# Performance work log

Measured on AMD Instinct MI355X. Metric: run time of the kernel, lower is better.

## Reference

```python
import jax, jax.numpy as jnp
import numpy as np

N = 4096        # batch nodes
E = 65536       # random edges (self-loops appended -> 69632 total)
F_IN = 256
H = 128
C = 2
MIN = 1024      # minority (class 1) count; first MIN nodes
REP = 2         # int(N_pct/100) synthetic reps per minority sample


def setup_inputs() -> dict:
    key = jax.random.key(0)
    ks = jax.random.split(key, 24)
    feat = jax.random.normal(ks[0], (N, F_IN), dtype=jnp.float32)
    src = jax.random.randint(ks[1], (E,), 0, N, dtype=jnp.int32)
    dst = jax.random.randint(ks[2], (E,), 0, N, dtype=jnp.int32)
    loops = jnp.arange(N, dtype=jnp.int32)
    src = jnp.concatenate([src, loops])
    dst = jnp.concatenate([dst, loops])
    # dense batch adjacency (target for EdgeLoss), A[i,j]=1 if edge j->i
    adj = jnp.zeros((N, N), dtype=jnp.float32).at[dst, src].set(1.0)
    # deterministic labels: first MIN nodes are minority class 1
    labels = jnp.concatenate([jnp.ones((MIN,), jnp.int32), jnp.zeros((N - MIN,), jnp.int32)])

    def w(k, shape, fan_in):
        return jax.random.normal(k, shape, dtype=jnp.float32) / np.sqrt(fan_in)

    params = dict(
        W_pool0=w(ks[3], (F_IN, F_IN), F_IN), b_pool0=jnp.zeros((F_IN,), jnp.float32),
        W_self0=w(ks[4], (H, F_IN), F_IN), W_neigh0=w(ks[5], (H, F_IN), F_IN), b0=jnp.zeros((H,), jnp.float32),
        W_pool1=w(ks[6], (H, H), H), b_pool1=jnp.zeros((H,), jnp.float32),
        W_self1=w(ks[7], (H, H), H), W_neigh1=w(ks[8], (H, H), H), b1=jnp.zeros((H,), jnp.float32),
        de_weight=jax.random.uniform(ks[9], (H, H), jnp.float32, -1.0 / np.sqrt(H), 1.0 / np.sqrt(H)),
        W_conv=w(ks[10], (H, 2 * H), 2 * H),
        W_clf=w(ks[11], (C, H), H), b_clf=jnp.zeros((C,), jnp.float32),
        gaps=jax.random.uniform(ks[12], (MIN, REP), jnp.float32),  # SMOTE interpolation gaps
    )
    return dict(feat=feat, adj=adj, src=src, dst=dst, labels=labels, **params)


def _sage_pool_layer(h, src, dst, W_pool, b_pool, W_self, W_neigh, b):
    # DGL SAGEConv aggregator_type='pool': max over neighbors of relu(fc_pool(h))
    p = jax.nn.relu(h @ W_pool.T + b_pool)                     # [N, d]
    hn = jax.ops.segment_max(p[src], dst, num_segments=h.shape[0])
    hn = jnp.where(jnp.isfinite(hn), hn, 0.0)
    return h @ W_self.T + hn @ W_neigh.T + b


def _l2norm(x, eps=1e-12):
    return x / jnp.maximum(jnp.linalg.norm(x, axis=1, keepdims=True), eps)


def _smote_nn_interp(cand, gaps):
    # pairwise euclidean distances (vectorized form of the per-row loop)
    sq = jnp.sum(cand * cand, axis=1)
    d2 = sq[:, None] + sq[None, :] - 2.0 * (cand @ cand.T)
    dist = jnp.sqrt(jnp.maximum(d2, 0.0))
    nn_idx = jnp.argsort(dist, axis=1)[:, 1]                   # k=2 -> single nearest (excl. self)
    diff = cand[nn_idx] - cand                                  # [MIN, H]
    synth = cand[:, None, :] + gaps[:, :, None] * diff[:, None, :]  # [MIN, REP, H], i-major order
    return synth.reshape(MIN * REP, cand.shape[1])


def reference(feat, adj, src, dst, labels,
              W_pool0, b_pool0, W_self0, W_neigh0, b0,
              W_pool1, b_pool1, W_self1, W_neigh1, b1,
              de_weight, W_conv, W_clf, b_clf, gaps):
    # ---- Encoder (2 SAGEConv 'pool' layers; dropout is eval-mode identity) ----
    h = _sage_pool_layer(feat, src, dst, W_pool0, b_pool0, W_self0, W_neigh0, b0)
    h = _l2norm(jax.nn.relu(h))
    h = _sage_pool_layer(h, src, dst, W_pool1, b_pool1, W_self1, W_neigh1, b1)
    # ---- SMOTE (minority = first MIN rows, by deterministic label construction) ----
    synth = _smote_nn_interp(h[:MIN], gaps)
    x = jnp.concatenate([h, synth], axis=0)                    # [N + MIN*REP, H]
    y = jnp.concatenate([labels, jnp.ones((MIN * REP,), jnp.int32)])
    # ---- Decoder: sigmoid(out @ out.T) ----
    out = x @ de_weight.T
    pred_adj = jax.nn.sigmoid(out @ out.T)                     # [6144, 6144]
    # ---- EdgeLoss vs dense batch adjacency ----
    rec = pred_adj[:N, :N]
    edge_num = jnp.sum(adj != 0).astype(jnp.float32)
    neg_w = edge_num / (float(N * N) - edge_num)
    weight = jnp.where(adj == 0, neg_w, 1.0)
    loss = jnp.sum(weight * (rec - adj) ** 2)
    # ---- threshold + SageClassifier (1 layer, no activation before clf) ----
    pred_adj = jnp.where(pred_adj >= 0.5, pred_adj, 0.0)
    neigh = (pred_adj @ x) / (jnp.sum(pred_adj, axis=1, keepdims=True) + 1.0)
    hc = jnp.concatenate([x, neigh], axis=-1) @ W_conv.T
    logits = hc @ W_clf.T + b_clf                              # [6144, 2]
    return logits, y, loss
```

## Files before the change

kernel.cpp:

```cpp
#include <hip/hip_runtime.h>
#include <cstddef>

typedef unsigned short ushort_t;
typedef __attribute__((ext_vector_type(8))) short bf16x8;
typedef __attribute__((ext_vector_type(4))) float f32x4;
typedef __attribute__((ext_vector_type(16))) float f32x16;

#define WS_P0     0u
#define WS_DOTS   0u
#define WS_OBK    524288u
#define WS_HN0    1048576u
#define WS_BITMAP 1048576u
#define WS_HC     1048576u
#define WS_H1     2097152u
#define WS_H1N    2621440u
#define WS_P1     3145728u
#define WS_PVB    3145728u
#define WS_HN1    3670016u
#define WS_H2     4194304u
#define WS_X      4718592u
#define WS_OB     5505024u
#define WS_NEIGH  6291456u
#define WS_ROWSUM 7077888u
#define WS_SCAL   7084032u
#define WS_DEG    7084048u
#define WS_NN     7088144u
#define WS_CUR    7089168u
#define WS_ROWPTR 7093264u
#define WS_EIDX   7097361u

__device__ inline ushort_t f2bf(float f) {
  unsigned u = __float_as_uint(f);
  u += 0x7fff + ((u >> 16) & 1);
  return (ushort_t)(u >> 16);
}

__global__ __launch_bounds__(256, 2) void gemm_nt(
    const float* __restrict__ A, int lda,
    const float* __restrict__ B, int ldb,
    const float* __restrict__ A2, int lda2,
    const float* __restrict__ B2, int ldb2,
    const float* __restrict__ bias,
    float* __restrict__ C, int ldc,
    int K, int relu,
    ushort_t* __restrict__ Cb,
    const float* __restrict__ a2scale,
    const float* __restrict__ Ahi)
{
  __shared__ float As[16][68];
  __shared__ float Bs[16][68];
  const int tid = threadIdx.x;
  const int tx = tid & 15, ty = tid >> 4;
  const int lr = tid >> 2;
  const int lk = (tid & 3) << 2;
  const int i0 = blockIdx.y << 6;
  const int j0 = blockIdx.x << 6;
  float acc[4][4] = {};
  const int npass = (A2 != nullptr) ? 2 : 1;
  for (int pass = 0; pass < npass; ++pass) {
    const float* Ap = pass ? A2 : A; const int la = pass ? lda2 : lda;
    const float* Bp = pass ? B2 : B; const int lb = pass ? ldb2 : ldb;
    const float sc = (pass && a2scale) ? __frcp_rn(a2scale[i0 + lr] + 1.f) : 1.f;
    const float* Arow = (pass == 0 && Ahi != nullptr && i0 >= 4096)
        ? (Ahi + (size_t)(i0 - 4096 + lr) * la)
        : (Ap + (size_t)(i0 + lr) * la);
    for (int k0 = 0; k0 < K; k0 += 16) {
      float4 ag = *(const float4*)(Arow + (k0 + lk));
      const float4 bg = *(const float4*)(Bp + (size_t)(j0 + lr) * lb + (k0 + lk));
      ag.x *= sc; ag.y *= sc; ag.z *= sc; ag.w *= sc;
      __syncthreads();
      As[lk+0][lr]=ag.x; As[lk+1][lr]=ag.y; As[lk+2][lr]=ag.z; As[lk+3][lr]=ag.w;
      Bs[lk+0][lr]=bg.x; Bs[lk+1][lr]=bg.y; Bs[lk+2][lr]=bg.z; Bs[lk+3][lr]=bg.w;
      __syncthreads();
#pragma unroll
      for (int k = 0; k < 16; ++k) {
        const float4 a4 = *(const float4*)&As[k][ty << 2];
        const float4 b4 = *(const float4*)&Bs[k][tx << 2];
        const float aa[4] = {a4.x, a4.y, a4.z, a4.w};
        const float bb[4] = {b4.x, b4.y, b4.z, b4.w};
#pragma unroll
        for (int ii = 0; ii < 4; ++ii)
#pragma unroll
          for (int jj = 0; jj < 4; ++jj)
            acc[ii][jj] += aa[ii] * bb[jj];
      }
    }
  }
  float badd[4] = {0.f, 0.f, 0.f, 0.f};
  if (bias) {
    const float4 t = *(const float4*)(bias + j0 + (tx << 2));
    badd[0]=t.x; badd[1]=t.y; badd[2]=t.z; badd[3]=t.w;
  }
#pragma unroll
  for (int ii = 0; ii < 4; ++ii) {
    float4 o;
    o.x = acc[ii][0] + badd[0];
    o.y = acc[ii][1] + badd[1];
    o.z = acc[ii][2] + badd[2];
    o.w = acc[ii][3] + badd[3];
    if (relu) { o.x=fmaxf(o.x,0.f); o.y=fmaxf(o.y,0.f); o.z=fmaxf(o.z,0.f); o.w=fmaxf(o.w,0.f); }
    if (Cb) {
      const int i_ = i0 + (ty << 2) + ii;
      const int j_ = j0 + (tx << 2);
      const size_t off = ((size_t)(i_ >> 5) << 12) +
                         (size_t)(((j_ >> 4) << 9) +
                                  ((((( j_ >> 3) & 1) << 5) + (i_ & 31)) << 3) +
                                  (j_ & 7));
      ushort4 ob4;
      ob4.x = f2bf(o.x); ob4.y = f2bf(o.y); ob4.z = f2bf(o.z); ob4.w = f2bf(o.w);
      *(ushort4*)(Cb + off) = ob4;
    } else {
      const size_t off = (size_t)(i0 + (ty<<2) + ii) * ldc + j0 + (tx<<2);
      *(float4*)(C + off) = o;
    }
  }
}

__global__ void count_k(const int* __restrict__ dst, int* __restrict__ deg, int E) {
  const int e = blockIdx.x * 256 + threadIdx.x;
  if (e < E) atomicAdd(&deg[dst[e]], 1);
}

__global__ __launch_bounds__(1024) void scan_k(const int* __restrict__ deg,
                                               int* __restrict__ rowptr,
                                               int* __restrict__ cursor) {
  __shared__ int sums[1024];
  const int t = threadIdx.x;
  const int4 d = *(const int4*)(deg + (t << 2));
  const int local = d.x + d.y + d.z + d.w;
  sums[t] = local;
  __syncthreads();
  for (int off = 1; off < 1024; off <<= 1) {
    int v = (t >= off) ? sums[t - off] : 0;
    __syncthreads();
    sums[t] += v;
    __syncthreads();
  }
  const int excl = sums[t] - local;
  const int o0 = excl, o1 = o0 + d.x, o2 = o1 + d.y, o3 = o2 + d.z;
  rowptr[(t<<2)+0]=o0; rowptr[(t<<2)+1]=o1; rowptr[(t<<2)+2]=o2; rowptr[(t<<2)+3]=o3;
  cursor[(t<<2)+0]=o0; cursor[(t<<2)+1]=o1; cursor[(t<<2)+2]=o2; cursor[(t<<2)+3]=o3;
  if (t == 1023) rowptr[4096] = sums[1023];
}

__global__ void fill_k(const int* __restrict__ src, const int* __restrict__ dst,
                       int* __restrict__ cursor, int* __restrict__ eidx, int E) {
  const int e = blockIdx.x * 256 + threadIdx.x;
  if (e < E) {
    const int p = atomicAdd(&cursor[dst[e]], 1);
    eidx[p] = src[e];
  }
}

__global__ void bitmap_build_k(const int* __restrict__ src, const int* __restrict__ dst,
                               unsigned* __restrict__ bitmap, int E) {
  const int e = blockIdx.x * 256 + threadIdx.x;
  if (e < E) {
    const unsigned cell = ((unsigned)dst[e] << 12) + (unsigned)src[e];
    atomicOr(&bitmap[cell >> 5], 1u << (cell & 31));
  }
}

__global__ void segmax_k(const float* __restrict__ p, const int* __restrict__ rowptr,
                         const int* __restrict__ eidx, float* __restrict__ hn, int F) {
  const int row = blockIdx.x, f = threadIdx.x;
  const int b = rowptr[row], e = rowptr[row + 1];
  float m = 0.f;
  for (int k = b; k < e; ++k) m = fmaxf(m, p[(size_t)eidx[k] * F + f]);
  hn[(size_t)row * F + f] = m;
}

__device__ inline float wave_sum(float v) {
#pragma unroll
  for (int o = 32; o > 0; o >>= 1) v += __shfl_down(v, o, 64);
  return v;
}

__global__ void relu_l2norm_k(const float* __restrict__ in, float* __restrict__ out,
                              unsigned* __restrict__ bitmap) {
  const int row = blockIdx.x, f = threadIdx.x;
  bitmap[(blockIdx.x << 7) + f] = 0u;
  const float v = fmaxf(in[(size_t)row * 128 + f], 0.f);
  const float ss = wave_sum(v * v);
  __shared__ float w[2];
  if ((f & 63) == 0) w[f >> 6] = ss;
  __syncthreads();
  const float denom = fmaxf(sqrtf(w[0] + w[1]), 1e-12f);
  out[(size_t)row * 128 + f] = v / denom;
}

__global__ void argmin_k(const float* __restrict__ dots, int* __restrict__ nn) {
  __shared__ float sqd[1024];
  const int i = blockIdx.x, tid = threadIdx.x;
#pragma unroll
  for (int z = 0; z < 4; ++z) {
    const int j = (tid << 2) + z;
    sqd[j] = dots[(size_t)j * 1025];
  }
  __syncthreads();
  float best = 3.402823466e38f; int bidx = 0x7fffffff;
  const float si = sqd[i];
  for (int j = tid; j < 1024; j += 256) {
    if (j == i) continue;
    float d2 = si + sqd[j] - 2.f * dots[(size_t)i * 1024 + j];
    d2 = fmaxf(d2, 0.f);
    if (d2 < best || (d2 == best && j < bidx)) { best = d2; bidx = j; }
  }
  __shared__ float bv[256]; __shared__ int bi[256];
  bv[tid] = best; bi[tid] = bidx;
  __syncthreads();
  for (int s = 128; s > 0; s >>= 1) {
    if (tid < s) {
      if (bv[tid+s] < bv[tid] || (bv[tid+s] == bv[tid] && bi[tid+s] < bi[tid])) {
        bv[tid] = bv[tid+s]; bi[tid] = bi[tid+s];
      }
    }
    __syncthreads();
  }
  if (tid == 0) nn[i] = bi[0];
}

__global__ __launch_bounds__(256) void build_pack_k(
    const float* __restrict__ h2, const int* __restrict__ nn,
    const float* __restrict__ gaps, float* __restrict__ synth,
    ushort_t* __restrict__ pvb) {
  __shared__ ushort_t s[4096];
  const int jt = blockIdx.x, tid = threadIdx.x;
  if (jt < 128) {
    const float* ip = h2 + ((size_t)jt << 12);
#pragma unroll
    for (int k = 0; k < 4; ++k) {
      const float4 v = *(const float4*)(ip + (tid << 4) + (k << 2));
      ushort4 h; h.x = f2bf(v.x); h.y = f2bf(v.y); h.z = f2bf(v.z); h.w = f2bf(v.w);
      *(ushort4*)(s + (tid << 4) + (k << 2)) = h;
    }
  } else {
    const int row = tid >> 3;
    const int sIdx = ((jt - 128) << 5) + row;
    const int i = sIdx >> 1;
    const float g = gaps[sIdx];
    const int ni = nn[i];
#pragma unroll
    for (int k = 0; k < 4; ++k) {
      const int f = ((tid & 7) << 4) + (k << 2);
      const float4 c4 = *(const float4*)(h2 + (size_t)i * 128 + f);
      const float4 n4 = *(const float4*)(h2 + (size_t)ni * 128 + f);
      float4 v;
      v.x = c4.x + g * (n4.x - c4.x);
      v.y = c4.y + g * (n4.y - c4.y);
      v.z = c4.z + g * (n4.z - c4.z);
      v.w = c4.w + g * (n4.w - c4.w);
      *(float4*)(synth + (size_t)sIdx * 128 + f) = v;
      ushort4 h; h.x = f2bf(v.x); h.y = f2bf(v.y); h.z = f2bf(v.z); h.w = f2bf(v.w);
      *(ushort4*)(s + (row << 7) + f) = h;
    }
  }
  __syncthreads();
  const int u = tid & 31, ft = (tid >> 5) & 3, cc = tid >> 7;
  ushort_t* op = pvb + ((size_t)jt << 12) + (cc << 11) + (ft << 9);
#pragma unroll
  for (int m = 0; m < 2; ++m) {
    const int l = (u << 1) + m;
    const int f = (ft << 5) + (l & 31);
    const int jb = (cc << 4) + ((l >> 5) << 3);
    ushort4 o0, o1;
    o0.x = s[(jb + 0) * 128 + f]; o0.y = s[(jb + 1) * 128 + f];
    o0.z = s[(jb + 2) * 128 + f]; o0.w = s[(jb + 3) * 128 + f];
    o1.x = s[(jb + 4) * 128 + f]; o1.y = s[(jb + 5) * 128 + f];
    o1.z = s[(jb + 6) * 128 + f]; o1.w = s[(jb + 7) * 128 + f];
    *(ushort4*)(op + (l << 3) + 0) = o0;
    *(ushort4*)(op + (l << 3) + 4) = o1;
  }
}

__global__ __launch_bounds__(256, 2) void fused_mfma(
    const ushort_t* __restrict__ obk,
    const ushort_t* __restrict__ pvb,
    const unsigned* __restrict__ bitmap,
    float* __restrict__ neigh,
    float* __restrict__ rowsum,
    float* __restrict__ scal)
{
  __shared__ float wred[4][4];
  const int tid = threadIdx.x;
  const int w = tid >> 6;
  const int lane = tid & 63;
  const int lo = lane & 31, hi = lane >> 5;
  const int it = (blockIdx.x << 2) + w;
  const int iw = it << 5;
  const int jt0 = blockIdx.y << 4;
  const bool loss_i = (it < 128);

  bf16x8 qf[8];
  {
    const ushort_t* qp = obk + ((size_t)it << 12) + (lane << 3);
#pragma unroll
    for (int c = 0; c < 8; ++c) qf[c] = *(const bf16x8*)(qp + (c << 9));
  }
  f32x16 oacc[4];
#pragma unroll
  for (int ft = 0; ft < 4; ++ft)
#pragma unroll
    for (int r = 0; r < 16; ++r) oacc[ft][r] = 0.f;
  float rs = 0.f, s_all = 0.f, s1a = 0.f, suba = 0.f, ecf = 0.f;

  bf16x8 a[8];
  {
    const ushort_t* kp = obk + ((size_t)jt0 << 12) + (lane << 3);
#pragma unroll
    for (int c = 0; c < 8; ++c) a[c] = *(const bf16x8*)(kp + (c << 9));
  }

  for (int t = 0; t < 16; ++t) {
    const int jt = jt0 + t;
    f32x16 s0, s1;
#pragma unroll
    for (int r = 0; r < 16; ++r) { s0[r] = 0.f; s1[r] = 0.f; }
#pragma unroll
    for (int c = 0; c < 4; ++c) {
      s0 = __builtin_amdgcn_mfma_f32_32x32x16_bf16(a[c], qf[c], s0, 0, 0, 0);
      s1 = __builtin_amdgcn_mfma_f32_32x32x16_bf16(a[c + 4], qf[c + 4], s1, 0, 0, 0);
    }
    bf16x8 bvf[2][4];
    {
      const ushort_t* vp = pvb + ((size_t)jt << 12) + (lane << 3);
#pragma unroll
      for (int cc = 0; cc < 2; ++cc)
#pragma unroll
        for (int ft = 0; ft < 4; ++ft)
          bvf[cc][ft] = *(const bf16x8*)(vp + (cc << 11) + (ft << 9));
    }
    if (t < 15) {
      const ushort_t* kp = obk + ((size_t)(jt + 1) << 12) + (lane << 3);
#pragma unroll
      for (int c = 0; c < 8; ++c) a[c] = *(const bf16x8*)(kp + (c << 9));
    }
    const bool loss_t = loss_i && (jt < 128);
    unsigned word = 0u;
    if (loss_t) word = bitmap[((unsigned)(iw + lo) << 7) + (unsigned)jt];
    float p[16];
    if (loss_t) {
      ecf += (float)__popc(word & (0x0F0F0F0Fu << (hi << 2)));
#pragma unroll
      for (int r = 0; r < 16; ++r) {
        const float v = s0[r] + s1[r];
        const float sg = __builtin_amdgcn_rcpf(1.f + __expf(-v));
        const int jl = (r & 3) + ((r >> 2) << 3) + (hi << 2);
        const float e_ = (float)((word >> jl) & 1u);
        s_all += sg * sg;
        s1a  += e_ * (sg - 1.f) * (sg - 1.f);
        suba += e_ * sg * sg;
        const float tv = (v >= 0.f) ? sg : 0.f;
        p[r] = tv; rs += tv;
      }
    } else {
#pragma unroll
      for (int r = 0; r < 16; ++r) {
        const float v = s0[r] + s1[r];
        const float sg = __builtin_amdgcn_rcpf(1.f + __expf(-v));
        const float tv = (v >= 0.f) ? sg : 0.f;
        p[r] = tv; rs += tv;
      }
    }
#pragma unroll
    for (int cc = 0; cc < 2; ++cc) {
      const int b8 = cc << 3;
      unsigned c01, c23, c45, c67;
      asm("v_cvt_pk_bf16_f32 %0, %1, %2" : "=v"(c01) : "v"(p[b8+0]), "v"(p[b8+1]));
      asm("v_cvt_pk_bf16_f32 %0, %1, %2" : "=v"(c23) : "v"(p[b8+2]), "v"(p[b8+3]));
      asm("v_cvt_pk_bf16_f32 %0, %1, %2" : "=v"(c45) : "v"(p[b8+4]), "v"(p[b8+5]));
      asm("v_cvt_pk_bf16_f32 %0, %1, %2" : "=v"(c67) : "v"(p[b8+6]), "v"(p[b8+7]));
      const auto w0 = __builtin_amdgcn_permlane32_swap((int)c01, (int)c45, false, false);
      const auto w1 = __builtin_amdgcn_permlane32_swap((int)c23, (int)c67, false, false);
      union { int i[4]; bf16x8 h; } u;
      u.i[0] = w0[0]; u.i[1] = w1[0]; u.i[2] = w0[1]; u.i[3] = w1[1];
#pragma unroll
      for (int ft = 0; ft < 4; ++ft)
        oacc[ft] = __builtin_amdgcn_mfma_f32_32x32x16_bf16(u.h, bvf[cc][ft], oacc[ft], 0, 0, 0);
    }
  }
#pragma unroll
  for (int ft = 0; ft < 4; ++ft)
#pragma unroll
    for (int r = 0; r < 16; ++r) {
      const int ir = (r & 3) + ((r >> 2) << 3) + (hi << 2);
      atomicAdd(&neigh[(size_t)(iw + ir) * 128 + (ft << 5) + lo], oacc[ft][r]);
    }
  rs += __shfl_xor(rs, 32, 64);
  if (hi == 0) atomicAdd(&rowsum[iw + lo], rs);
  {
    float v0 = wave_sum(s_all), v1 = wave_sum(s1a), v2 = wave_sum(suba), v3 = wave_sum(ecf);
    if (lane == 0) { wred[w][0] = v0; wred[w][1] = v1; wred[w][2] = v2; wred[w][3] = v3; }
  }
  __syncthreads();
  if (tid < 4) {
    const float t = wred[0][tid] + wred[1][tid] + wred[2][tid] + wred[3][tid];
    const int dst = (tid == 0) ? 0 : (tid == 1) ? 1 : (tid == 2) ? 3 : 4;
    atomicAdd(&scal[dst], t);
  }
}

__global__ void logits_y_loss_k(const float* __restrict__ hc, const float* __restrict__ Wclf,
                                const float* __restrict__ bclf, const int* __restrict__ labels,
                                const float* __restrict__ scal,
                                float* __restrict__ outp) {
  const int i = blockIdx.x, f = threadIdx.x;
  const float h = hc[(size_t)i * 128 + f];
  const float v0 = wave_sum(h * Wclf[f]);
  const float v1 = wave_sum(h * Wclf[128 + f]);
  __shared__ float w0[2], w1[2];
  if ((f & 63) == 0) { w0[f >> 6] = v0; w1[f >> 6] = v1; }
  __syncthreads();
  if (f == 0) {
    outp[(size_t)i * 2 + 0] = w0[0] + w0[1] + bclf[0];
    outp[(size_t)i * 2 + 1] = w1[0] + w1[1] + bclf[1];
    outp[12288 + i] = (i < 4096) ? (float)labels[i] : 1.f;
    if (i == 0) {
      const float cnt = scal[4];
      const float neg_w = cnt / (16777216.f - cnt);
      outp[18432] = neg_w * (scal[0] - scal[3]) + scal[1];
    }
  }
}

extern "C" void kernel_launch(void* const* d_in, const int* in_sizes, int n_in,
                              void* d_out, int out_size, void* d_ws, size_t ws_size,
                              hipStream_t stream) {
  const float* feat     = (const float*)d_in[0];
  const int*   src      = (const int*)d_in[2];
  const int*   dst      = (const int*)d_in[3];
  const int*   labels   = (const int*)d_in[4];
  const float* W_pool0  = (const float*)d_in[5];
  const float* b_pool0  = (const float*)d_in[6];
  const float* W_self0  = (const float*)d_in[7];
  const float* W_neigh0 = (const float*)d_in[8];
  const float* b0       = (const float*)d_in[9];
  const float* W_pool1  = (const float*)d_in[10];
  const float* b_pool1  = (const float*)d_in[11];
  const float* W_self1  = (const float*)d_in[12];
  const float* W_neigh1 = (const float*)d_in[13];
  const float* b1       = (const float*)d_in[14];
  const float* de_w     = (const float*)d_in[15];
  const float* W_conv   = (const float*)d_in[16];
  const float* W_clf    = (const float*)d_in[17];
  const float* b_clf    = (const float*)d_in[18];
  const float* gaps     = (const float*)d_in[19];
  const int E = in_sizes[2];

  float* ws = (float*)d_ws;
  float* p0       = ws + WS_P0;
  float* dots     = ws + WS_DOTS;
  ushort_t* obk   = (ushort_t*)(ws + WS_OBK);
  float* hn0      = ws + WS_HN0;
  unsigned* bitmap= (unsigned*)(ws + WS_BITMAP);
  float* hc       = ws + WS_HC;
  float* h1       = ws + WS_H1;
  float* h1n      = ws + WS_H1N;
  float* p1       = ws + WS_P1;
  ushort_t* pvb   = (ushort_t*)(ws + WS_PVB);
  float* hn1      = ws + WS_HN1;
  float* h2       = ws + WS_H2;
  float* synth    = ws + WS_X;
  float* neigh    = ws + WS_NEIGH;
  float* rowsum   = ws + WS_ROWSUM;
  float* scal     = ws + WS_SCAL;
  int* deg        = (int*)(ws + WS_DEG);
  int* nn         = (int*)(ws + WS_NN);
  int* cursor     = (int*)(ws + WS_CUR);
  int* rowptr     = (int*)(ws + WS_ROWPTR);
  int* eidx       = (int*)(ws + WS_EIDX);

  float* outp = (float*)d_out;
  const dim3 blk(256);

  hipMemsetAsync(neigh, 0, (size_t)(WS_DEG + 4096 - WS_NEIGH) * 4, stream);

  count_k<<<(E + 255) / 256, blk, 0, stream>>>(dst, deg, E);
  scan_k<<<1, 1024, 0, stream>>>(deg, rowptr, cursor);
  fill_k<<<(E + 255) / 256, blk, 0, stream>>>(src, dst, cursor, eidx, E);

  gemm_nt<<<dim3(4, 64), blk, 0, stream>>>(feat, 256, W_pool0, 256,
                                           nullptr, 0, nullptr, 0,
                                           b_pool0, p0, 256, 256, 1, nullptr, nullptr, nullptr);
  segmax_k<<<4096, 256, 0, stream>>>(p0, rowptr, eidx, hn0, 256);
  gemm_nt<<<dim3(2, 64), blk, 0, stream>>>(feat, 256, W_self0, 256,
                                           hn0, 256, W_neigh0, 256,
                                           b0, h1, 128, 256, 0, nullptr, nullptr, nullptr);
  relu_l2norm_k<<<4096, 128, 0, stream>>>(h1, h1n, bitmap);
  bitmap_build_k<<<(E + 255) / 256, blk, 0, stream>>>(src, dst, bitmap, E);

  gemm_nt<<<dim3(2, 64), blk, 0, stream>>>(h1n, 128, W_pool1, 128,
                                           nullptr, 0, nullptr, 0,
                                           b_pool1, p1, 128, 128, 1, nullptr, nullptr, nullptr);
  segmax_k<<<4096, 128, 0, stream>>>(p1, rowptr, eidx, hn1, 128);
  gemm_nt<<<dim3(2, 64), blk, 0, stream>>>(h1n, 128, W_self1, 128,
                                           hn1, 128, W_neigh1, 128,
                                           b1, h2, 128, 128, 0, nullptr, nullptr, nullptr);

  gemm_nt<<<dim3(16, 16), blk, 0, stream>>>(h2, 128, h2, 128,
                                            nullptr, 0, nullptr, 0,
                                            nullptr, dots, 1024, 128, 0, nullptr, nullptr, nullptr);
  argmin_k<<<1024, 256, 0, stream>>>(dots, nn);
  build_pack_k<<<192, blk, 0, stream>>>(h2, nn, gaps, synth, pvb);

  gemm_nt<<<dim3(2, 96), blk, 0, stream>>>(h2, 128, de_w, 128,
                                           nullptr, 0, nullptr, 0,
                                           nullptr, nullptr, 0, 128, 0, obk, nullptr, synth);
  fused_mfma<<<dim3(48, 12), blk, 0, stream>>>(obk, pvb, bitmap, neigh, rowsum, scal);

  gemm_nt<<<dim3(2, 96), blk, 0, stream>>>(h2, 128, W_conv, 256,
                                           neigh, 128, W_conv + 128, 256,
                                           nullptr, hc, 128, 128, 0, nullptr, rowsum, synth);
  logits_y_loss_k<<<6144, 128, 0, stream>>>(hc, W_clf, b_clf, labels, scal, outp);

  (void)n_in; (void)out_size; (void)ws_size; (void)in_sizes;
}
```

Before: 339.5 us.

## Fuse bitmap build into degree count and software-pipeline decoder score MFMAs

The adjacency bitmap gets its own workspace region, is zeroed by the existing memset, and is built inside the degree-count kernel. This removes one kernel launch and the zeroing inside relu_l2norm. In the fused decoder/aggregation kernel, the QK score MFMAs for tile t+1 are issued before the sigmoid and PV work of tile t, and K loads are prefetched two tiles ahead. The intent is to overlap matrix work with the elementwise epilogue, at the cost of more live registers. The memset now covers a larger range.

```diff
diff --git a/kernel.cpp b/kernel.cpp
--- a/kernel.cpp
+++ b/kernel.cpp
@@ -10,7 +10,6 @@
 #define WS_DOTS   0u
 #define WS_OBK    524288u
 #define WS_HN0    1048576u
-#define WS_BITMAP 1048576u
 #define WS_HC     1048576u
 #define WS_H1     2097152u
 #define WS_H1N    2621440u
@@ -19,7 +18,7 @@
 #define WS_HN1    3670016u
 #define WS_H2     4194304u
 #define WS_X      4718592u
-#define WS_OB     5505024u
+#define WS_BITMAP 5767168u
 #define WS_NEIGH  6291456u
 #define WS_ROWSUM 7077888u
 #define WS_SCAL   7084032u
@@ -116,9 +115,15 @@
   }
 }
 
-__global__ void count_k(const int* __restrict__ dst, int* __restrict__ deg, int E) {
+__global__ void count_bitmap_k(const int* __restrict__ src, const int* __restrict__ dst,
+                               int* __restrict__ deg, unsigned* __restrict__ bitmap, int E) {
   const int e = blockIdx.x * 256 + threadIdx.x;
-  if (e < E) atomicAdd(&deg[dst[e]], 1);
+  if (e < E) {
+    const int d_ = dst[e], s_ = src[e];
+    atomicAdd(&deg[d_], 1);
+    const unsigned cell = ((unsigned)d_ << 12) + (unsigned)s_;
+    atomicOr(&bitmap[cell >> 5], 1u << (cell & 31));
+  }
 }
 
 __global__ __launch_bounds__(1024) void scan_k(const int* __restrict__ deg,
@@ -152,15 +157,6 @@
   }
 }
 
-__global__ void bitmap_build_k(const int* __restrict__ src, const int* __restrict__ dst,
-                               unsigned* __restrict__ bitmap, int E) {
-  const int e = blockIdx.x * 256 + threadIdx.x;
-  if (e < E) {
-    const unsigned cell = ((unsigned)dst[e] << 12) + (unsigned)src[e];
-    atomicOr(&bitmap[cell >> 5], 1u << (cell & 31));
-  }
-}
-
 __global__ void segmax_k(const float* __restrict__ p, const int* __restrict__ rowptr,
                          const int* __restrict__ eidx, float* __restrict__ hn, int F) {
   const int row = blockIdx.x, f = threadIdx.x;
@@ -176,10 +172,8 @@
   return v;
 }
 
-__global__ void relu_l2norm_k(const float* __restrict__ in, float* __restrict__ out,
-                              unsigned* __restrict__ bitmap) {
+__global__ void relu_l2norm_k(const float* __restrict__ in, float* __restrict__ out) {
   const int row = blockIdx.x, f = threadIdx.x;
-  bitmap[(blockIdx.x << 7) + f] = 0u;
   const float v = fmaxf(in[(size_t)row * 128 + f], 0.f);
   const float ss = wave_sum(v * v);
   __shared__ float w[2];
@@ -310,17 +304,20 @@
 #pragma unroll
     for (int c = 0; c < 8; ++c) a[c] = *(const bf16x8*)(kp + (c << 9));
   }
+  f32x16 sp;
+#pragma unroll
+  for (int r = 0; r < 16; ++r) sp[r] = 0.f;
+#pragma unroll
+  for (int c = 0; c < 8; ++c)
+    sp = __builtin_amdgcn_mfma_f32_32x32x16_bf16(a[c], qf[c], sp, 0, 0, 0);
+  {
+    const ushort_t* kp = obk + ((size_t)(jt0 + 1) << 12) + (lane << 3);
+#pragma unroll
+    for (int c = 0; c < 8; ++c) a[c] = *(const bf16x8*)(kp + (c << 9));
+  }
 
   for (int t = 0; t < 16; ++t) {
     const int jt = jt0 + t;
-    f32x16 s0, s1;
-#pragma unroll
-    for (int r = 0; r < 16; ++r) { s0[r] = 0.f; s1[r] = 0.f; }
-#pragma unroll
-    for (int c = 0; c < 4; ++c) {
-      s0 = __builtin_amdgcn_mfma_f32_32x32x16_bf16(a[c], qf[c], s0, 0, 0, 0);
-      s1 = __builtin_amdgcn_mfma_f32_32x32x16_bf16(a[c + 4], qf[c + 4], s1, 0, 0, 0);
-    }
     bf16x8 bvf[2][4];
     {
       const ushort_t* vp = pvb + ((size_t)jt << 12) + (lane << 3);
@@ -330,8 +327,16 @@
         for (int ft = 0; ft < 4; ++ft)
           bvf[cc][ft] = *(const bf16x8*)(vp + (cc << 11) + (ft << 9));
     }
+    f32x16 sn;
+#pragma unroll
+    for (int r = 0; r < 16; ++r) sn[r] = 0.f;
     if (t < 15) {
-      const ushort_t* kp = obk + ((size_t)(jt + 1) << 12) + (lane << 3);
+#pragma unroll
+      for (int c = 0; c < 8; ++c)
+        sn = __builtin_amdgcn_mfma_f32_32x32x16_bf16(a[c], qf[c], sn, 0, 0, 0);
+    }
+    if (t < 14) {
+      const ushort_t* kp = obk + ((size_t)(jt + 2) << 12) + (lane << 3);
 #pragma unroll
       for (int c = 0; c < 8; ++c) a[c] = *(const bf16x8*)(kp + (c << 9));
     }
@@ -343,7 +348,7 @@
       ecf += (float)__popc(word & (0x0F0F0F0Fu << (hi << 2)));
 #pragma unroll
       for (int r = 0; r < 16; ++r) {
-        const float v = s0[r] + s1[r];
+        const float v = sp[r];
         const float sg = __builtin_amdgcn_rcpf(1.f + __expf(-v));
         const int jl = (r & 3) + ((r >> 2) << 3) + (hi << 2);
         const float e_ = (float)((word >> jl) & 1u);
@@ -356,7 +361,7 @@
     } else {
 #pragma unroll
       for (int r = 0; r < 16; ++r) {
-        const float v = s0[r] + s1[r];
+        const float v = sp[r];
         const float sg = __builtin_amdgcn_rcpf(1.f + __expf(-v));
         const float tv = (v >= 0.f) ? sg : 0.f;
         p[r] = tv; rs += tv;
@@ -378,6 +383,7 @@
       for (int ft = 0; ft < 4; ++ft)
         oacc[ft] = __builtin_amdgcn_mfma_f32_32x32x16_bf16(u.h, bvf[cc][ft], oacc[ft], 0, 0, 0);
     }
+    sp = sn;
   }
 #pragma unroll
   for (int ft = 0; ft < 4; ++ft)
@@ -473,9 +479,9 @@
   float* outp = (float*)d_out;
   const dim3 blk(256);
 
-  hipMemsetAsync(neigh, 0, (size_t)(WS_DEG + 4096 - WS_NEIGH) * 4, stream);
-
-  count_k<<<(E + 255) / 256, blk, 0, stream>>>(dst, deg, E);
+  hipMemsetAsync(bitmap, 0, (size_t)(WS_DEG + 4096 - WS_BITMAP) * 4, stream);
+
+  count_bitmap_k<<<(E + 255) / 256, blk, 0, stream>>>(src, dst, deg, bitmap, E);
   scan_k<<<1, 1024, 0, stream>>>(deg, rowptr, cursor);
   fill_k<<<(E + 255) / 256, blk, 0, stream>>>(src, dst, cursor, eidx, E);
 
@@ -486,8 +492,7 @@
   gemm_nt<<<dim3(2, 64), blk, 0, stream>>>(feat, 256, W_self0, 256,
                                            hn0, 256, W_neigh0, 256,
                                            b0, h1, 128, 256, 0, nullptr, nullptr, nullptr);
-  relu_l2norm_k<<<4096, 128, 0, stream>>>(h1, h1n, bitmap);
-  bitmap_build_k<<<(E + 255) / 256, blk, 0, stream>>>(src, dst, bitmap, E);
+  relu_l2norm_k<<<4096, 128, 0, stream>>>(h1, h1n);
 
   gemm_nt<<<dim3(2, 64), blk, 0, stream>>>(h1n, 128, W_pool1, 128,
                                            nullptr, 0, nullptr, 0,
```

Result: slower. 357.2 us (+5.2%).

## Fuse CSR build, layer-1 epilogue, and conv+classifier into fewer kernels

Applied to the files above, without the earlier changes.

Replaces the count/scan/fill/bitmap kernels with one single-block kernel that builds degrees in shared memory, scans them, fills the CSR and sets the adjacency bitmap. It fuses the layer-0 output GEMM with ReLU, L2 normalisation and the layer-1 pool GEMM in one kernel, and fuses the conv GEMM with the classifier logits. This cuts launches and intermediate global traffic. The risk is that a single 1024-thread block handling all 69632 edges with global atomics serialises work that previously ran across many blocks.

```diff
diff --git a/kernel.cpp b/kernel.cpp
--- a/kernel.cpp
+++ b/kernel.cpp
@@ -10,22 +10,18 @@
 #define WS_DOTS   0u
 #define WS_OBK    524288u
 #define WS_HN0    1048576u
-#define WS_BITMAP 1048576u
-#define WS_HC     1048576u
-#define WS_H1     2097152u
 #define WS_H1N    2621440u
 #define WS_P1     3145728u
 #define WS_PVB    3145728u
 #define WS_HN1    3670016u
 #define WS_H2     4194304u
 #define WS_X      4718592u
-#define WS_OB     5505024u
+#define WS_BITMAP 5767168u
 #define WS_NEIGH  6291456u
 #define WS_ROWSUM 7077888u
 #define WS_SCAL   7084032u
 #define WS_DEG    7084048u
 #define WS_NN     7088144u
-#define WS_CUR    7089168u
 #define WS_ROWPTR 7093264u
 #define WS_EIDX   7097361u
 
@@ -116,18 +112,41 @@
   }
 }
 
-__global__ void count_k(const int* __restrict__ dst, int* __restrict__ deg, int E) {
-  const int e = blockIdx.x * 256 + threadIdx.x;
-  if (e < E) atomicAdd(&deg[dst[e]], 1);
-}
-
-__global__ __launch_bounds__(1024) void scan_k(const int* __restrict__ deg,
-                                               int* __restrict__ rowptr,
-                                               int* __restrict__ cursor) {
+__global__ __launch_bounds__(1024) void csr_k(
+    const int* __restrict__ src, const int* __restrict__ dst,
+    unsigned* __restrict__ bitmap, int* __restrict__ rowptr,
+    int* __restrict__ eidx, int E)
+{
+  __shared__ int degL[4096];
   __shared__ int sums[1024];
   const int t = threadIdx.x;
-  const int4 d = *(const int4*)(deg + (t << 2));
-  const int local = d.x + d.y + d.z + d.w;
+#pragma unroll
+  for (int z = 0; z < 4; ++z) degL[(z << 10) + t] = 0;
+  __syncthreads();
+  const int nIt = E >> 12;
+  for (int r = 0; r < nIt; ++r) {
+    const int base = ((r << 10) + t) << 2;
+    const int4 d4 = *(const int4*)(dst + base);
+    const int4 s4 = *(const int4*)(src + base);
+    atomicAdd(&degL[d4.x], 1);
+    atomicAdd(&degL[d4.y], 1);
+    atomicAdd(&degL[d4.z], 1);
+    atomicAdd(&degL[d4.w], 1);
+    unsigned c;
+    c = ((unsigned)d4.x << 12) + (unsigned)s4.x; atomicOr(&bitmap[c >> 5], 1u << (c & 31));
+    c = ((unsigned)d4.y << 12) + (unsigned)s4.y; atomicOr(&bitmap[c >> 5], 1u << (c & 31));
+    c = ((unsigned)d4.z << 12) + (unsigned)s4.z; atomicOr(&bitmap[c >> 5], 1u << (c & 31));
+    c = ((unsigned)d4.w << 12) + (unsigned)s4.w; atomicOr(&bitmap[c >> 5], 1u << (c & 31));
+  }
+  for (int e = (nIt << 12) + t; e < E; e += 1024) {
+    const int d_ = dst[e], s_ = src[e];
+    atomicAdd(&degL[d_], 1);
+    const unsigned c = ((unsigned)d_ << 12) + (unsigned)s_;
+    atomicOr(&bitmap[c >> 5], 1u << (c & 31));
+  }
+  __syncthreads();
+  const int dx = degL[(t<<2)+0], dy = degL[(t<<2)+1], dz = degL[(t<<2)+2], dw = degL[(t<<2)+3];
+  const int local = dx + dy + dz + dw;
   sums[t] = local;
   __syncthreads();
   for (int off = 1; off < 1024; off <<= 1) {
@@ -137,27 +156,23 @@
     __syncthreads();
   }
   const int excl = sums[t] - local;
-  const int o0 = excl, o1 = o0 + d.x, o2 = o1 + d.y, o3 = o2 + d.z;
+  const int o0 = excl, o1 = o0 + dx, o2 = o1 + dy, o3 = o2 + dz;
   rowptr[(t<<2)+0]=o0; rowptr[(t<<2)+1]=o1; rowptr[(t<<2)+2]=o2; rowptr[(t<<2)+3]=o3;
-  cursor[(t<<2)+0]=o0; cursor[(t<<2)+1]=o1; cursor[(t<<2)+2]=o2; cursor[(t<<2)+3]=o3;
+  degL[(t<<2)+0]=o0; degL[(t<<2)+1]=o1; degL[(t<<2)+2]=o2; degL[(t<<2)+3]=o3;
   if (t == 1023) rowptr[4096] = sums[1023];
-}
-
-__global__ void fill_k(const int* __restrict__ src, const int* __restrict__ dst,
-                       int* __restrict__ cursor, int* __restrict__ eidx, int E) {
-  const int e = blockIdx.x * 256 + threadIdx.x;
-  if (e < E) {
-    const int p = atomicAdd(&cursor[dst[e]], 1);
-    eidx[p] = src[e];
-  }
-}
-
-__global__ void bitmap_build_k(const int* __restrict__ src, const int* __restrict__ dst,
-                               unsigned* __restrict__ bitmap, int E) {
-  const int e = blockIdx.x * 256 + threadIdx.x;
-  if (e < E) {
-    const unsigned cell = ((unsigned)dst[e] << 12) + (unsigned)src[e];
-    atomicOr(&bitmap[cell >> 5], 1u << (cell & 31));
+  __syncthreads();
+  for (int r = 0; r < nIt; ++r) {
+    const int base = ((r << 10) + t) << 2;
+    const int4 d4 = *(const int4*)(dst + base);
+    const int4 s4 = *(const int4*)(src + base);
+    int p;
+    p = atomicAdd(&degL[d4.x], 1); eidx[p] = s4.x;
+    p = atomicAdd(&degL[d4.y], 1); eidx[p] = s4.y;
+    p = atomicAdd(&degL[d4.z], 1); eidx[p] = s4.z;
+    p = atomicAdd(&degL[d4.w], 1); eidx[p] = s4.w;
+  }
+  for (int e = (nIt << 12) + t; e < E; e += 1024) {
+    const int p = atomicAdd(&degL[dst[e]], 1); eidx[p] = src[e];
   }
 }
 
@@ -176,17 +191,107 @@
   return v;
 }
 
-__global__ void relu_l2norm_k(const float* __restrict__ in, float* __restrict__ out,
-                              unsigned* __restrict__ bitmap) {
-  const int row = blockIdx.x, f = threadIdx.x;
-  bitmap[(blockIdx.x << 7) + f] = 0u;
-  const float v = fmaxf(in[(size_t)row * 128 + f], 0.f);
-  const float ss = wave_sum(v * v);
-  __shared__ float w[2];
-  if ((f & 63) == 0) w[f >> 6] = ss;
-  __syncthreads();
-  const float denom = fmaxf(sqrtf(w[0] + w[1]), 1e-12f);
-  out[(size_t)row * 128 + f] = v / denom;
+__global__ __launch_bounds__(256) void layer1_k(
+    const float* __restrict__ feat, const float* __restrict__ hn0,
+    const float* __restrict__ Wself, const float* __restrict__ Wneigh,
+    const float* __restrict__ b0,
+    const float* __restrict__ Wpool1, const float* __restrict__ bpool1,
+    float* __restrict__ h1n, float* __restrict__ p1)
+{
+  __shared__ float As[16][34];
+  __shared__ float Bs[16][132];
+  __shared__ float hS[128][33];
+  __shared__ float red[32][17];
+  __shared__ float dnm[32];
+  const int tid = threadIdx.x;
+  const int tx = tid & 15, ty = tid >> 4;
+  const int r0 = ty << 1, r1 = r0 + 1;
+  const int i0 = blockIdx.x << 5;
+  const int lr = tid >> 3, lk2 = (tid & 7) << 1;
+  const int jr = tid >> 1, jk = (tid & 1) << 3;
+  float acc[2][8] = {};
+  for (int pass = 0; pass < 2; ++pass) {
+    const float* Ap = pass ? hn0 : feat;
+    const float* Bp = pass ? Wneigh : Wself;
+    for (int k0 = 0; k0 < 256; k0 += 16) {
+      const float2 a2 = *(const float2*)(Ap + (size_t)(i0 + lr) * 256 + k0 + lk2);
+      float4 bg0 = *(const float4*)(Bp + (size_t)jr * 256 + k0 + jk);
+      float4 bg1 = *(const float4*)(Bp + (size_t)jr * 256 + k0 + jk + 4);
+      __syncthreads();
+      As[lk2][lr] = a2.x; As[lk2 + 1][lr] = a2.y;
+      Bs[jk+0][jr]=bg0.x; Bs[jk+1][jr]=bg0.y; Bs[jk+2][jr]=bg0.z; Bs[jk+3][jr]=bg0.w;
+      Bs[jk+4][jr]=bg1.x; Bs[jk+5][jr]=bg1.y; Bs[jk+6][jr]=bg1.z; Bs[jk+7][jr]=bg1.w;
+      __syncthreads();
+#pragma unroll
+      for (int k = 0; k < 16; ++k) {
+        const float a0 = As[k][r0], a1 = As[k][r1];
+        const float4 b0v = *(const float4*)&Bs[k][tx << 3];
+        const float4 b1v = *(const float4*)&Bs[k][(tx << 3) + 4];
+        const float bb[8] = {b0v.x,b0v.y,b0v.z,b0v.w,b1v.x,b1v.y,b1v.z,b1v.w};
+#pragma unroll
+        for (int jj = 0; jj < 8; ++jj) { acc[0][jj] += a0 * bb[jj]; acc[1][jj] += a1 * bb[jj]; }
+      }
+    }
+  }
+  float ss0 = 0.f, ss1 = 0.f;
+#pragma unroll
+  for (int jj = 0; jj < 8; ++jj) {
+    const float bvj = b0[(tx << 3) + jj];
+    acc[0][jj] = fmaxf(acc[0][jj] + bvj, 0.f); ss0 += acc[0][jj] * acc[0][jj];
+    acc[1][jj] = fmaxf(acc[1][jj] + bvj, 0.f); ss1 += acc[1][jj] * acc[1][jj];
+  }
+  red[r0][tx] = ss0; red[r1][tx] = ss1;
+  __syncthreads();
+  if (tid < 32) {
+    float s = 0.f;
+#pragma unroll
+    for (int u = 0; u < 16; ++u) s += red[tid][u];
+    dnm[tid] = fmaxf(sqrtf(s), 1e-12f);
+  }
+  __syncthreads();
+  const float d0 = dnm[r0], d1 = dnm[r1];
+#pragma unroll
+  for (int jj = 0; jj < 8; ++jj) { acc[0][jj] /= d0; acc[1][jj] /= d1; }
+#pragma unroll
+  for (int ii = 0; ii < 2; ++ii) {
+    const int row = r0 + ii;
+    const float4 w0 = {acc[ii][0],acc[ii][1],acc[ii][2],acc[ii][3]};
+    const float4 w1 = {acc[ii][4],acc[ii][5],acc[ii][6],acc[ii][7]};
+    *(float4*)(h1n + (size_t)(i0 + row) * 128 + (tx << 3)) = w0;
+    *(float4*)(h1n + (size_t)(i0 + row) * 128 + (tx << 3) + 4) = w1;
+#pragma unroll
+    for (int jj = 0; jj < 8; ++jj) hS[(tx << 3) + jj][row] = acc[ii][jj];
+  }
+  __syncthreads();
+  float ac2[2][8] = {};
+  for (int k0 = 0; k0 < 128; k0 += 16) {
+    float4 bg0 = *(const float4*)(Wpool1 + (size_t)jr * 128 + k0 + jk);
+    float4 bg1 = *(const float4*)(Wpool1 + (size_t)jr * 128 + k0 + jk + 4);
+    __syncthreads();
+    Bs[jk+0][jr]=bg0.x; Bs[jk+1][jr]=bg0.y; Bs[jk+2][jr]=bg0.z; Bs[jk+3][jr]=bg0.w;
+    Bs[jk+4][jr]=bg1.x; Bs[jk+5][jr]=bg1.y; Bs[jk+6][jr]=bg1.z; Bs[jk+7][jr]=bg1.w;
+    __syncthreads();
+#pragma unroll
+    for (int k = 0; k < 16; ++k) {
+      const float a0 = hS[k0 + k][r0], a1 = hS[k0 + k][r1];
+      const float4 b0v = *(const float4*)&Bs[k][tx << 3];
+      const float4 b1v = *(const float4*)&Bs[k][(tx << 3) + 4];
+      const float bb[8] = {b0v.x,b0v.y,b0v.z,b0v.w,b1v.x,b1v.y,b1v.z,b1v.w};
+#pragma unroll
+      for (int jj = 0; jj < 8; ++jj) { ac2[0][jj] += a0 * bb[jj]; ac2[1][jj] += a1 * bb[jj]; }
+    }
+  }
+#pragma unroll
+  for (int ii = 0; ii < 2; ++ii) {
+    float o[8];
+#pragma unroll
+    for (int jj = 0; jj < 8; ++jj)
+      o[jj] = fmaxf(ac2[ii][jj] + bpool1[(tx << 3) + jj], 0.f);
+    const float4 w0 = {o[0],o[1],o[2],o[3]};
+    const float4 w1 = {o[4],o[5],o[6],o[7]};
+    *(float4*)(p1 + (size_t)(i0 + r0 + ii) * 128 + (tx << 3)) = w0;
+    *(float4*)(p1 + (size_t)(i0 + r0 + ii) * 128 + (tx << 3) + 4) = w1;
+  }
 }
 
 __global__ void argmin_k(const float* __restrict__ dots, int* __restrict__ nn) {
@@ -400,26 +505,84 @@
   }
 }
 
-__global__ void logits_y_loss_k(const float* __restrict__ hc, const float* __restrict__ Wclf,
-                                const float* __restrict__ bclf, const int* __restrict__ labels,
-                                const float* __restrict__ scal,
-                                float* __restrict__ outp) {
-  const int i = blockIdx.x, f = threadIdx.x;
-  const float h = hc[(size_t)i * 128 + f];
-  const float v0 = wave_sum(h * Wclf[f]);
-  const float v1 = wave_sum(h * Wclf[128 + f]);
-  __shared__ float w0[2], w1[2];
-  if ((f & 63) == 0) { w0[f >> 6] = v0; w1[f >> 6] = v1; }
-  __syncthreads();
-  if (f == 0) {
-    outp[(size_t)i * 2 + 0] = w0[0] + w0[1] + bclf[0];
-    outp[(size_t)i * 2 + 1] = w1[0] + w1[1] + bclf[1];
+__global__ __launch_bounds__(256) void conv_logits_k(
+    const float* __restrict__ h2, const float* __restrict__ synth,
+    const float* __restrict__ neigh, const float* __restrict__ rowsum,
+    const float* __restrict__ Wconv,
+    const float* __restrict__ Wclf,
+    const float* __restrict__ bclf,
+    const int* __restrict__ labels,
+    const float* __restrict__ scal,
+    float* __restrict__ outp)
+{
+  __shared__ float As[16][34];
+  __shared__ float Bs[16][132];
+  __shared__ float scale[32];
+  __shared__ float wc[2][128];
+  __shared__ float red[2][32][17];
+  const int tid = threadIdx.x;
+  const int tx = tid & 15, ty = tid >> 4;
+  const int r0 = ty << 1, r1 = r0 + 1;
+  const int i0 = blockIdx.x << 5;
+  const int lr = tid >> 3, lk2 = (tid & 7) << 1;
+  const int jr = tid >> 1, jk = (tid & 1) << 3;
+  if (tid < 32) scale[tid] = __frcp_rn(rowsum[i0 + tid] + 1.f);
+  wc[tid >> 7][tid & 127] = Wclf[tid];
+  const float* Abase = (i0 < 4096) ? (h2 + (size_t)i0 * 128)
+                                   : (synth + (size_t)(i0 - 4096) * 128);
+  float acc[2][8] = {};
+  for (int pass = 0; pass < 2; ++pass) {
+    const float* Bp = Wconv + (pass ? 128 : 0);
+    for (int k0 = 0; k0 < 128; k0 += 16) {
+      float2 a2;
+      if (pass == 0) {
+        a2 = *(const float2*)(Abase + (size_t)lr * 128 + k0 + lk2);
+      } else {
+        a2 = *(const float2*)(neigh + (size_t)(i0 + lr) * 128 + k0 + lk2);
+        const float sc = scale[lr];
+        a2.x *= sc; a2.y *= sc;
+      }
+      float4 bg0 = *(const float4*)(Bp + (size_t)jr * 256 + k0 + jk);
+      float4 bg1 = *(const float4*)(Bp + (size_t)jr * 256 + k0 + jk + 4);
+      __syncthreads();
+      As[lk2][lr] = a2.x; As[lk2 + 1][lr] = a2.y;
+      Bs[jk+0][jr]=bg0.x; Bs[jk+1][jr]=bg0.y; Bs[jk+2][jr]=bg0.z; Bs[jk+3][jr]=bg0.w;
+      Bs[jk+4][jr]=bg1.x; Bs[jk+5][jr]=bg1.y; Bs[jk+6][jr]=bg1.z; Bs[jk+7][jr]=bg1.w;
+      __syncthreads();
+#pragma unroll
+      for (int k = 0; k < 16; ++k) {
+        const float a0 = As[k][r0], a1 = As[k][r1];
+        const float4 b0v = *(const float4*)&Bs[k][tx << 3];
+        const float4 b1v = *(const float4*)&Bs[k][(tx << 3) + 4];
+        const float bb[8] = {b0v.x,b0v.y,b0v.z,b0v.w,b1v.x,b1v.y,b1v.z,b1v.w};
+#pragma unroll
+        for (int jj = 0; jj < 8; ++jj) { acc[0][jj] += a0 * bb[jj]; acc[1][jj] += a1 * bb[jj]; }
+      }
+    }
+  }
+  float l00 = 0.f, l01 = 0.f, l10 = 0.f, l11 = 0.f;
+#pragma unroll
+  for (int jj = 0; jj < 8; ++jj) {
+    const float w0_ = wc[0][(tx << 3) + jj], w1_ = wc[1][(tx << 3) + jj];
+    l00 += acc[0][jj] * w0_; l01 += acc[0][jj] * w1_;
+    l10 += acc[1][jj] * w0_; l11 += acc[1][jj] * w1_;
+  }
+  red[0][r0][tx] = l00; red[1][r0][tx] = l01;
+  red[0][r1][tx] = l10; red[1][r1][tx] = l11;
+  __syncthreads();
+  if (tid < 32) {
+    float s0 = 0.f, s1 = 0.f;
+#pragma unroll
+    for (int u = 0; u < 16; ++u) { s0 += red[0][tid][u]; s1 += red[1][tid][u]; }
+    const int i = i0 + tid;
+    outp[(size_t)i * 2 + 0] = s0 + bclf[0];
+    outp[(size_t)i * 2 + 1] = s1 + bclf[1];
     outp[12288 + i] = (i < 4096) ? (float)labels[i] : 1.f;
-    if (i == 0) {
-      const float cnt = scal[4];
-      const float neg_w = cnt / (16777216.f - cnt);
-      outp[18432] = neg_w * (scal[0] - scal[3]) + scal[1];
-    }
+  }
+  if (blockIdx.x == 0 && tid == 0) {
+    const float cnt = scal[4];
+    const float neg_w = cnt / (16777216.f - cnt);
+    outp[18432] = neg_w * (scal[0] - scal[3]) + scal[1];
   }
 }
 
@@ -453,8 +616,6 @@
   ushort_t* obk   = (ushort_t*)(ws + WS_OBK);
   float* hn0      = ws + WS_HN0;
   unsigned* bitmap= (unsigned*)(ws + WS_BITMAP);
-  float* hc       = ws + WS_HC;
-  float* h1       = ws + WS_H1;
   float* h1n      = ws + WS_H1N;
   float* p1       = ws + WS_P1;
   ushort_t* pvb   = (ushort_t*)(ws + WS_PVB);
@@ -464,34 +625,24 @@
   float* neigh    = ws + WS_NEIGH;
   float* rowsum   = ws + WS_ROWSUM;
   float* scal     = ws + WS_SCAL;
-  int* deg        = (int*)(ws + WS_DEG);
   int* nn         = (int*)(ws + WS_NN);
-  int* cursor     = (int*)(ws + WS_CUR);
   int* rowptr     = (int*)(ws + WS_ROWPTR);
   int* eidx       = (int*)(ws + WS_EIDX);
 
   float* outp = (float*)d_out;
   const dim3 blk(256);
 
-  hipMemsetAsync(neigh, 0, (size_t)(WS_DEG + 4096 - WS_NEIGH) * 4, stream);
-
-  count_k<<<(E + 255) / 256, blk, 0, stream>>>(dst, deg, E);
-  scan_k<<<1, 1024, 0, stream>>>(deg, rowptr, cursor);
-  fill_k<<<(E + 255) / 256, blk, 0, stream>>>(src, dst, cursor, eidx, E);
+  hipMemsetAsync(bitmap, 0, (size_t)(WS_DEG - WS_BITMAP) * 4, stream);
+
+  csr_k<<<1, 1024, 0, stream>>>(src, dst, bitmap, rowptr, eidx, E);
 
   gemm_nt<<<dim3(4, 64), blk, 0, stream>>>(feat, 256, W_pool0, 256,
                                            nullptr, 0, nullptr, 0,
                                            b_pool0, p0, 256, 256, 1, nullptr, nullptr, nullptr);
   segmax_k<<<4096, 256, 0, stream>>>(p0, rowptr, eidx, hn0, 256);
-  gemm_nt<<<dim3(2, 64), blk, 0, stream>>>(feat, 256, W_self0, 256,
-                                           hn0, 256, W_neigh0, 256,
-                                           b0, h1, 128, 256, 0, nullptr, nullptr, nullptr);
-  relu_l2norm_k<<<4096, 128, 0, stream>>>(h1, h1n, bitmap);
-  bitmap_build_k<<<(E + 255) / 256, blk, 0, stream>>>(src, dst, bitmap, E);
-
-  gemm_nt<<<dim3(2, 64), blk, 0, stream>>>(h1n, 128, W_pool1, 128,
-                                           nullptr, 0, nullptr, 0,
-                                           b_pool1, p1, 128, 128, 1, nullptr, nullptr, nullptr);
+  layer1_k<<<128, blk, 0, stream>>>(feat, hn0, W_self0, W_neigh0, b0,
+                                    W_pool1, b_pool1, h1n, p1);
+
   segmax_k<<<4096, 128, 0, stream>>>(p1, rowptr, eidx, hn1, 128);
   gemm_nt<<<dim3(2, 64), blk, 0, stream>>>(h1n, 128, W_self1, 128,
                                            hn1, 128, W_neigh1, 128,
@@ -508,10 +659,8 @@
                                            nullptr, nullptr, 0, 128, 0, obk, nullptr, synth);
   fused_mfma<<<dim3(48, 12), blk, 0, stream>>>(obk, pvb, bitmap, neigh, rowsum, scal);
 
-  gemm_nt<<<dim3(2, 96), blk, 0, stream>>>(h2, 128, W_conv, 256,
-                                           neigh, 128, W_conv + 128, 256,
-                                           nullptr, hc, 128, 128, 0, nullptr, rowsum, synth);
-  logits_y_loss_k<<<6144, 128, 0, stream>>>(hc, W_clf, b_clf, labels, scal, outp);
+  conv_logits_k<<<192, blk, 0, stream>>>(h2, synth, neigh, rowsum,
+                                         W_conv, W_clf, b_clf, labels, scal, outp);
 
   (void)n_in; (void)out_size; (void)ws_size; (void)in_sizes;
 }
```

New measurement: 491.3 us. 1.45x slower.
